# Optimization experiments

Hardware: AMD Instinct MI355X
Metric: run time of the kernel (lower is better)

Reference implementation:

```python
import jax, jax.numpy as jnp
import numpy as np

D_MODEL = 1024
D_STATE = 16
BATCH = 4
SEQLEN = 4096


def setup_inputs() -> dict:
    key = jax.random.key(0)
    kx, kA, kB, kC = jax.random.split(key, 4)
    x = jax.random.normal(kx, (BATCH, SEQLEN, D_MODEL), dtype=jnp.float32)
    # Params per init_weights(): A ~ N(-0.5, 0.1), B ~ N(0, 0.1), C ~ N(0, 0.1), D = 0
    A = -0.5 + 0.1 * jax.random.normal(kA, (1, D_STATE), dtype=jnp.float32)
    B_in = 0.1 * jax.random.normal(kB, (D_MODEL, D_STATE), dtype=jnp.float32)
    C = 0.1 * jax.random.normal(kC, (D_STATE, D_MODEL), dtype=jnp.float32)
    D = jnp.zeros((D_MODEL,), dtype=jnp.float32)
    return {"x": x, "A": A, "B_in": B_in, "C": C, "D": D}


def reference(x, A, B_in, C, D):
    # x: [B, N, E]; A: [1, S]; B_in: [E, S]; C: [S, E]; D: [E]
    A_neg = -jnp.exp(A)                              # [1, S]
    Bx = jnp.einsum('bne,es->bns', x, B_in)          # [B, N, S] = x @ B
    delta = jax.nn.softplus(Bx)                      # softplus(u @ B)
    decay = jnp.exp(delta * A_neg)                   # [B, N, S]

    def step(h, inp):
        d_t, bx_t = inp                              # each [B, S]
        h = h * d_t + bx_t
        return h, h

    h0 = jnp.zeros((x.shape[0], A.shape[1]), dtype=x.dtype)
    # scan over time: inputs [N, B, S]
    _, hs = jax.lax.scan(step, h0, (decay.transpose(1, 0, 2), Bx.transpose(1, 0, 2)))
    # readout: y_t = h_t @ C + x_t * D  (dropout p=0.0 -> identity)
    y = jnp.einsum('nbs,se->bne', hs, C) + x * D
    return y
```

## Files before the change

kernel.cpp:

```cpp
#include <hip/hip_runtime.h>

#define NSEQ 4096
#define EDIM 1024

#define OFF_BXT  0u
#define OFF_DECT 262144u
#define OFF_HT   524288u

__device__ __forceinline__ void fma4(float4& a, float xv, const float4& b) {
    a.x = fmaf(xv, b.x, a.x);
    a.y = fmaf(xv, b.y, a.y);
    a.z = fmaf(xv, b.z, a.z);
    a.w = fmaf(xv, b.w, a.w);
}

__global__ __launch_bounds__(512) void k1_bx(const float* __restrict__ x,
                                             const float* __restrict__ A,
                                             const float* __restrict__ Bin,
                                             float* __restrict__ ws) {
    __shared__ float smem[8704];

    const int tid  = threadIdx.x;
    const int lane = tid & 63;
    const int wu   = __builtin_amdgcn_readfirstlane(tid) >> 6;
    const int r0   = blockIdx.x * 64;
    const int b    = r0 >> 12;
    const int n0   = r0 & 4095;

    const float4* xf4 = (const float4*)x;
    const float4* Bf4 = (const float4*)Bin;

    float acc[16];
#pragma unroll
    for (int s = 0; s < 16; s++) acc[s] = 0.f;

    float4 pf[4];
#pragma unroll
    for (int k = 0; k < 4; k++) {
        int i = tid + 512 * k, row = i >> 5, c4 = i & 31;
        pf[k] = xf4[(size_t)(r0 + row) * 256 + c4];
    }

    for (int c = 0; c < 8; ++c) {
        if (c) __syncthreads();
#pragma unroll
        for (int k = 0; k < 4; k++) {
            int i = tid + 512 * k, row = i >> 5, c4 = i & 31;
            float* p = &smem[row * 129 + c4 * 4];
            p[0] = pf[k].x; p[1] = pf[k].y; p[2] = pf[k].z; p[3] = pf[k].w;
        }
        if (c < 7) {
#pragma unroll
            for (int k = 0; k < 4; k++) {
                int i = tid + 512 * k, row = i >> 5, c4 = i & 31;
                pf[k] = xf4[(size_t)(r0 + row) * 256 + (c + 1) * 32 + c4];
            }
        }
        __syncthreads();

        const int eb = wu * 16;
#pragma unroll
        for (int j = 0; j < 16; ++j) {
            const int e = c * 128 + eb + j;
            const float4 b0 = Bf4[e * 4 + 0];
            const float4 b1 = Bf4[e * 4 + 1];
            const float4 b2 = Bf4[e * 4 + 2];
            const float4 b3 = Bf4[e * 4 + 3];
            const float xv = smem[lane * 129 + eb + j];
            acc[0]  = fmaf(xv, b0.x, acc[0]);  acc[1]  = fmaf(xv, b0.y, acc[1]);
            acc[2]  = fmaf(xv, b0.z, acc[2]);  acc[3]  = fmaf(xv, b0.w, acc[3]);
            acc[4]  = fmaf(xv, b1.x, acc[4]);  acc[5]  = fmaf(xv, b1.y, acc[5]);
            acc[6]  = fmaf(xv, b1.z, acc[6]);  acc[7]  = fmaf(xv, b1.w, acc[7]);
            acc[8]  = fmaf(xv, b2.x, acc[8]);  acc[9]  = fmaf(xv, b2.y, acc[9]);
            acc[10] = fmaf(xv, b2.z, acc[10]); acc[11] = fmaf(xv, b2.w, acc[11]);
            acc[12] = fmaf(xv, b3.x, acc[12]); acc[13] = fmaf(xv, b3.y, acc[13]);
            acc[14] = fmaf(xv, b3.z, acc[14]); acc[15] = fmaf(xv, b3.w, acc[15]);
        }
    }

    __syncthreads();
    {
        int base = (wu * 64 + lane) * 17;
#pragma unroll
        for (int s = 0; s < 16; s++) smem[base + s] = acc[s];
    }
    __syncthreads();

#pragma unroll
    for (int half = 0; half < 2; half++) {
        int o   = tid + half * 512;
        int s   = o >> 6;
        int row = o & 63;
        float v = 0.f;
#pragma unroll
        for (int w = 0; w < 8; w++) v += smem[(w * 64 + row) * 17 + s];
        float sp  = fmaxf(v, 0.f) + log1pf(expf(-fabsf(v)));
        float dec = expf(-expf(A[s]) * sp);
        size_t off = (size_t)(b * 16 + s) * NSEQ + n0 + row;
        ws[OFF_BXT + off]  = v;
        ws[OFF_DECT + off] = dec;
    }
}

__global__ __launch_bounds__(256) void k2_scan(float* __restrict__ ws) {
    __shared__ float sP[256], sH[256];
    const int tid   = threadIdx.x;
    const int chain = blockIdx.x;
    const size_t f4 = (size_t)chain * 1024 + tid * 4;

    const float4* Bx4 = (const float4*)(ws + OFF_BXT);
    const float4* De4 = (const float4*)(ws + OFF_DECT);
    float4 bx[4], de[4];
#pragma unroll
    for (int k = 0; k < 4; k++) { bx[k] = Bx4[f4 + k]; de[k] = De4[f4 + k]; }

    float P = 1.f, h = 0.f;
#pragma unroll
    for (int k = 0; k < 4; k++) {
        h = fmaf(h, de[k].x, bx[k].x); P *= de[k].x;
        h = fmaf(h, de[k].y, bx[k].y); P *= de[k].y;
        h = fmaf(h, de[k].z, bx[k].z); P *= de[k].z;
        h = fmaf(h, de[k].w, bx[k].w); P *= de[k].w;
    }

    sP[tid] = P; sH[tid] = h;
    __syncthreads();
    for (int off = 1; off < 256; off <<= 1) {
        float pp = 1.f, hp = 0.f;
        bool act = (tid >= off);
        if (act) { pp = sP[tid - off]; hp = sH[tid - off]; }
        float p = sP[tid], hh = sH[tid];
        __syncthreads();
        if (act) { sP[tid] = pp * p; sH[tid] = fmaf(hp, p, hh); }
        __syncthreads();
    }
    float hr = (tid > 0) ? sH[tid - 1] : 0.f;

    const int bb = chain >> 4, ss = chain & 15;
    float* ht = ws + OFF_HT + ((size_t)bb * NSEQ + tid * 16) * 16 + ss;
#pragma unroll
    for (int k = 0; k < 4; k++) {
        hr = fmaf(hr, de[k].x, bx[k].x); ht[(k * 4 + 0) * 16] = hr;
        hr = fmaf(hr, de[k].y, bx[k].y); ht[(k * 4 + 1) * 16] = hr;
        hr = fmaf(hr, de[k].z, bx[k].z); ht[(k * 4 + 2) * 16] = hr;
        hr = fmaf(hr, de[k].w, bx[k].w); ht[(k * 4 + 3) * 16] = hr;
    }
}

__global__ __launch_bounds__(256) void k3_out(const float* __restrict__ x,
                                              const float* __restrict__ C,
                                              const float* __restrict__ D,
                                              const float* __restrict__ ws,
                                              float* __restrict__ out) {
    const int tid = threadIdx.x;
    const int blk = blockIdx.x;
    const int tc  = blk & 255;
    const int b   = blk >> 8;
    const int t0  = tc * 16;

    const float4* C4 = (const float4*)C;
    float4 creg[16];
#pragma unroll
    for (int s = 0; s < 16; s++) creg[s] = C4[s * 256 + tid];
    float4 dreg = ((const float4*)D)[tid];

    const bool needX = __any((dreg.x != 0.f) | (dreg.y != 0.f) |
                             (dreg.z != 0.f) | (dreg.w != 0.f));

    const float* hb = ws + OFF_HT + ((size_t)b * NSEQ + t0) * 16;

    const float4* x4 = (const float4*)x;
    float4* o4 = (float4*)out;
    const size_t rowbase = ((size_t)b * NSEQ + t0) * 256;

    if (needX) {
#pragma unroll 4
        for (int tt = 0; tt < 16; tt++) {
            float4 xv = x4[rowbase + tt * 256 + tid];
            float4 y;
            y.x = xv.x * dreg.x; y.y = xv.y * dreg.y;
            y.z = xv.z * dreg.z; y.w = xv.w * dreg.w;
#pragma unroll
            for (int s = 0; s < 16; s++) fma4(y, hb[tt * 16 + s], creg[s]);
            o4[rowbase + tt * 256 + tid] = y;
        }
    } else {
#pragma unroll 4
        for (int tt = 0; tt < 16; tt++) {
            float4 y = make_float4(0.f, 0.f, 0.f, 0.f);
#pragma unroll
            for (int s = 0; s < 16; s++) fma4(y, hb[tt * 16 + s], creg[s]);
            o4[rowbase + tt * 256 + tid] = y;
        }
    }
}

extern "C" void kernel_launch(void* const* d_in, const int* in_sizes, int n_in,
                              void* d_out, int out_size, void* d_ws, size_t ws_size,
                              hipStream_t stream) {
    const float* x   = (const float*)d_in[0];
    const float* A   = (const float*)d_in[1];
    const float* Bin = (const float*)d_in[2];
    const float* C   = (const float*)d_in[3];
    const float* D   = (const float*)d_in[4];
    float* out = (float*)d_out;
    float* ws  = (float*)d_ws;

    hipLaunchKernelGGL(k1_bx,   dim3(256),  dim3(512), 0, stream, x, A, Bin, ws);
    hipLaunchKernelGGL(k2_scan, dim3(64),   dim3(256), 0, stream, ws);
    hipLaunchKernelGGL(k3_out,  dim3(1024), dim3(256), 0, stream, x, C, D, ws, out);
}
```

Before: 148.3 us.

## Split Bx GEMM over E halves, move softplus/decay into scan, shuffle-based scan

k1 now launches 512 blocks of 256 threads, each handling half of the E dimension for 64 rows. It uses double-buffered shared-memory staging with float4 stores and loads, and writes partial Bx sums to two workspace halves. k2 sums the halves, computes softplus and decay itself, and replaces the shared-memory Hillis-Steele scan with wave shuffles plus a small cross-wave combine, cutting the number of barriers. The aim is more parallelism in k1 and fewer barriers in k2, at the cost of an extra partial-sum write and read.

```diff
diff --git a/kernel.cpp b/kernel.cpp
--- a/kernel.cpp
+++ b/kernel.cpp
@@ -3,9 +3,8 @@
 #define NSEQ 4096
 #define EDIM 1024
 
-#define OFF_BXT  0u
-#define OFF_DECT 262144u
-#define OFF_HT   524288u
+#define OFF_PBX 0u
+#define OFF_HT  524288u
 
 __device__ __forceinline__ void fma4(float4& a, float xv, const float4& b) {
     a.x = fmaf(xv, b.x, a.x);
@@ -14,16 +13,16 @@
     a.w = fmaf(xv, b.w, a.w);
 }
 
-__global__ __launch_bounds__(512) void k1_bx(const float* __restrict__ x,
-                                             const float* __restrict__ A,
-                                             const float* __restrict__ Bin,
-                                             float* __restrict__ ws) {
-    __shared__ float smem[8704];
+__global__ __launch_bounds__(256, 2) void k1_bx(const float* __restrict__ x,
+                                                const float* __restrict__ Bin,
+                                                float* __restrict__ ws) {
+    __shared__ float smem[2 * 64 * 132];
 
     const int tid  = threadIdx.x;
     const int lane = tid & 63;
     const int wu   = __builtin_amdgcn_readfirstlane(tid) >> 6;
-    const int r0   = blockIdx.x * 64;
+    const int r0   = (blockIdx.x >> 1) * 64;
+    const int eh   = blockIdx.x & 1;
     const int b    = r0 >> 12;
     const int n0   = r0 & 4095;
 
@@ -34,116 +33,127 @@
 #pragma unroll
     for (int s = 0; s < 16; s++) acc[s] = 0.f;
 
-    float4 pf[4];
+    float4 pf[8];
+#pragma unroll
+    for (int k = 0; k < 8; k++) {
+        int i = tid + 256 * k, row = i >> 5, c4 = i & 31;
+        pf[k] = xf4[(size_t)(r0 + row) * 256 + eh * 128 + c4];
+    }
+
+    for (int c = 0; c < 4; ++c) {
+        float* stg = &smem[(c & 1) * 8448];
+#pragma unroll
+        for (int k = 0; k < 8; k++) {
+            int i = tid + 256 * k, row = i >> 5, c4 = i & 31;
+            *(float4*)&stg[row * 132 + c4 * 4] = pf[k];
+        }
+        if (c < 3) {
+#pragma unroll
+            for (int k = 0; k < 8; k++) {
+                int i = tid + 256 * k, row = i >> 5, c4 = i & 31;
+                pf[k] = xf4[(size_t)(r0 + row) * 256 + eh * 128 + (c + 1) * 32 + c4];
+            }
+        }
+        __syncthreads();
+
+#pragma unroll
+        for (int j4 = 0; j4 < 8; j4++) {
+            const float4 xq = *(const float4*)&stg[lane * 132 + wu * 32 + j4 * 4];
+#pragma unroll
+            for (int jj = 0; jj < 4; jj++) {
+                const int e = eh * 512 + c * 128 + wu * 32 + j4 * 4 + jj;
+                const float4 b0 = Bf4[e * 4 + 0];
+                const float4 b1 = Bf4[e * 4 + 1];
+                const float4 b2 = Bf4[e * 4 + 2];
+                const float4 b3 = Bf4[e * 4 + 3];
+                const float xv = (jj == 0) ? xq.x : (jj == 1) ? xq.y
+                                : (jj == 2) ? xq.z : xq.w;
+                acc[0]  = fmaf(xv, b0.x, acc[0]);  acc[1]  = fmaf(xv, b0.y, acc[1]);
+                acc[2]  = fmaf(xv, b0.z, acc[2]);  acc[3]  = fmaf(xv, b0.w, acc[3]);
+                acc[4]  = fmaf(xv, b1.x, acc[4]);  acc[5]  = fmaf(xv, b1.y, acc[5]);
+                acc[6]  = fmaf(xv, b1.z, acc[6]);  acc[7]  = fmaf(xv, b1.w, acc[7]);
+                acc[8]  = fmaf(xv, b2.x, acc[8]);  acc[9]  = fmaf(xv, b2.y, acc[9]);
+                acc[10] = fmaf(xv, b2.z, acc[10]); acc[11] = fmaf(xv, b2.w, acc[11]);
+                acc[12] = fmaf(xv, b3.x, acc[12]); acc[13] = fmaf(xv, b3.y, acc[13]);
+                acc[14] = fmaf(xv, b3.z, acc[14]); acc[15] = fmaf(xv, b3.w, acc[15]);
+            }
+        }
+        __syncthreads();
+    }
+
+    {
+        const int rb = (wu * 64 + lane) * 17;
+#pragma unroll
+        for (int s = 0; s < 16; s++) smem[rb + s] = acc[s];
+    }
+    __syncthreads();
+
+#pragma unroll
+    for (int q = 0; q < 4; q++) {
+        const int o   = tid + 256 * q;
+        const int s   = o >> 6;
+        const int row = o & 63;
+        const float v = smem[(0 * 64 + row) * 17 + s] + smem[(1 * 64 + row) * 17 + s] +
+                        smem[(2 * 64 + row) * 17 + s] + smem[(3 * 64 + row) * 17 + s];
+        ws[OFF_PBX + eh * 262144u + (size_t)(b * 16 + s) * NSEQ + n0 + row] = v;
+    }
+}
+
+__global__ __launch_bounds__(256) void k2_scan(const float* __restrict__ A,
+                                               float* __restrict__ ws) {
+    __shared__ float sP[4], sH[4];
+    const int tid   = threadIdx.x;
+    const int lane  = tid & 63;
+    const int w     = tid >> 6;
+    const int chain = blockIdx.x;
+    const int bb    = chain >> 4, ss = chain & 15;
+
+    const float4* P0 = (const float4*)(ws + OFF_PBX) + (size_t)chain * 1024;
+    const float4* P1 = (const float4*)(ws + OFF_PBX + 262144u) + (size_t)chain * 1024;
+
+    float bx[16], de[16];
+    const float Ae = expf(A[ss]);
 #pragma unroll
     for (int k = 0; k < 4; k++) {
-        int i = tid + 512 * k, row = i >> 5, c4 = i & 31;
-        pf[k] = xf4[(size_t)(r0 + row) * 256 + c4];
-    }
-
-    for (int c = 0; c < 8; ++c) {
-        if (c) __syncthreads();
-#pragma unroll
-        for (int k = 0; k < 4; k++) {
-            int i = tid + 512 * k, row = i >> 5, c4 = i & 31;
-            float* p = &smem[row * 129 + c4 * 4];
-            p[0] = pf[k].x; p[1] = pf[k].y; p[2] = pf[k].z; p[3] = pf[k].w;
-        }
-        if (c < 7) {
-#pragma unroll
-            for (int k = 0; k < 4; k++) {
-                int i = tid + 512 * k, row = i >> 5, c4 = i & 31;
-                pf[k] = xf4[(size_t)(r0 + row) * 256 + (c + 1) * 32 + c4];
-            }
-        }
-        __syncthreads();
-
-        const int eb = wu * 16;
-#pragma unroll
-        for (int j = 0; j < 16; ++j) {
-            const int e = c * 128 + eb + j;
-            const float4 b0 = Bf4[e * 4 + 0];
-            const float4 b1 = Bf4[e * 4 + 1];
-            const float4 b2 = Bf4[e * 4 + 2];
-            const float4 b3 = Bf4[e * 4 + 3];
-            const float xv = smem[lane * 129 + eb + j];
-            acc[0]  = fmaf(xv, b0.x, acc[0]);  acc[1]  = fmaf(xv, b0.y, acc[1]);
-            acc[2]  = fmaf(xv, b0.z, acc[2]);  acc[3]  = fmaf(xv, b0.w, acc[3]);
-            acc[4]  = fmaf(xv, b1.x, acc[4]);  acc[5]  = fmaf(xv, b1.y, acc[5]);
-            acc[6]  = fmaf(xv, b1.z, acc[6]);  acc[7]  = fmaf(xv, b1.w, acc[7]);
-            acc[8]  = fmaf(xv, b2.x, acc[8]);  acc[9]  = fmaf(xv, b2.y, acc[9]);
-            acc[10] = fmaf(xv, b2.z, acc[10]); acc[11] = fmaf(xv, b2.w, acc[11]);
-            acc[12] = fmaf(xv, b3.x, acc[12]); acc[13] = fmaf(xv, b3.y, acc[13]);
-            acc[14] = fmaf(xv, b3.z, acc[14]); acc[15] = fmaf(xv, b3.w, acc[15]);
-        }
-    }
-
+        float4 a0 = P0[tid * 4 + k], a1 = P1[tid * 4 + k];
+        float vv[4] = {a0.x + a1.x, a0.y + a1.y, a0.z + a1.z, a0.w + a1.w};
+#pragma unroll
+        for (int j = 0; j < 4; j++) {
+            float v  = vv[j];
+            float sp = fmaxf(v, 0.f) + log1pf(expf(-fabsf(v)));
+            bx[k * 4 + j] = v;
+            de[k * 4 + j] = expf(-Ae * sp);
+        }
+    }
+
+    float P = 1.f, h = 0.f;
+#pragma unroll
+    for (int k = 0; k < 16; k++) { h = fmaf(h, de[k], bx[k]); P *= de[k]; }
+
+    float Pi = P, hi = h;
+#pragma unroll
+    for (int off = 1; off < 64; off <<= 1) {
+        float Pp = __shfl_up(Pi, off, 64);
+        float hp = __shfl_up(hi, off, 64);
+        if (lane >= off) { hi = fmaf(hp, Pi, hi); Pi *= Pp; }
+    }
+
+    if (lane == 63) { sP[w] = Pi; sH[w] = hi; }
     __syncthreads();
-    {
-        int base = (wu * 64 + lane) * 17;
-#pragma unroll
-        for (int s = 0; s < 16; s++) smem[base + s] = acc[s];
-    }
-    __syncthreads();
-
-#pragma unroll
-    for (int half = 0; half < 2; half++) {
-        int o   = tid + half * 512;
-        int s   = o >> 6;
-        int row = o & 63;
-        float v = 0.f;
-#pragma unroll
-        for (int w = 0; w < 8; w++) v += smem[(w * 64 + row) * 17 + s];
-        float sp  = fmaxf(v, 0.f) + log1pf(expf(-fabsf(v)));
-        float dec = expf(-expf(A[s]) * sp);
-        size_t off = (size_t)(b * 16 + s) * NSEQ + n0 + row;
-        ws[OFF_BXT + off]  = v;
-        ws[OFF_DECT + off] = dec;
-    }
-}
-
-__global__ __launch_bounds__(256) void k2_scan(float* __restrict__ ws) {
-    __shared__ float sP[256], sH[256];
-    const int tid   = threadIdx.x;
-    const int chain = blockIdx.x;
-    const size_t f4 = (size_t)chain * 1024 + tid * 4;
-
-    const float4* Bx4 = (const float4*)(ws + OFF_BXT);
-    const float4* De4 = (const float4*)(ws + OFF_DECT);
-    float4 bx[4], de[4];
-#pragma unroll
-    for (int k = 0; k < 4; k++) { bx[k] = Bx4[f4 + k]; de[k] = De4[f4 + k]; }
-
-    float P = 1.f, h = 0.f;
-#pragma unroll
-    for (int k = 0; k < 4; k++) {
-        h = fmaf(h, de[k].x, bx[k].x); P *= de[k].x;
-        h = fmaf(h, de[k].y, bx[k].y); P *= de[k].y;
-        h = fmaf(h, de[k].z, bx[k].z); P *= de[k].z;
-        h = fmaf(h, de[k].w, bx[k].w); P *= de[k].w;
-    }
-
-    sP[tid] = P; sH[tid] = h;
-    __syncthreads();
-    for (int off = 1; off < 256; off <<= 1) {
-        float pp = 1.f, hp = 0.f;
-        bool act = (tid >= off);
-        if (act) { pp = sP[tid - off]; hp = sH[tid - off]; }
-        float p = sP[tid], hh = sH[tid];
-        __syncthreads();
-        if (act) { sP[tid] = pp * p; sH[tid] = fmaf(hp, p, hh); }
-        __syncthreads();
-    }
-    float hr = (tid > 0) ? sH[tid - 1] : 0.f;
-
-    const int bb = chain >> 4, ss = chain & 15;
-    float* ht = ws + OFF_HT + ((size_t)bb * NSEQ + tid * 16) * 16 + ss;
-#pragma unroll
-    for (int k = 0; k < 4; k++) {
-        hr = fmaf(hr, de[k].x, bx[k].x); ht[(k * 4 + 0) * 16] = hr;
-        hr = fmaf(hr, de[k].y, bx[k].y); ht[(k * 4 + 1) * 16] = hr;
-        hr = fmaf(hr, de[k].z, bx[k].z); ht[(k * 4 + 2) * 16] = hr;
-        hr = fmaf(hr, de[k].w, bx[k].w); ht[(k * 4 + 3) * 16] = hr;
+
+    float hw = 0.f;
+    for (int q = 0; q < w; q++) hw = fmaf(hw, sP[q], sH[q]);
+
+    float Pe = __shfl_up(Pi, 1, 64);
+    float he = __shfl_up(hi, 1, 64);
+    if (lane == 0) { Pe = 1.f; he = 0.f; }
+    float hr = fmaf(hw, Pe, he);
+
+    float* htp = ws + OFF_HT + ((size_t)bb * NSEQ + tid * 16) * 16 + ss;
+#pragma unroll
+    for (int k = 0; k < 16; k++) {
+        hr = fmaf(hr, de[k], bx[k]);
+        htp[k * 16] = hr;
     }
 }
 
@@ -206,7 +216,7 @@
     float* out = (float*)d_out;
     float* ws  = (float*)d_ws;
 
-    hipLaunchKernelGGL(k1_bx,   dim3(256),  dim3(512), 0, stream, x, A, Bin, ws);
-    hipLaunchKernelGGL(k2_scan, dim3(64),   dim3(256), 0, stream, ws);
+    hipLaunchKernelGGL(k1_bx,   dim3(512),  dim3(256), 0, stream, x, Bin, ws);
+    hipLaunchKernelGGL(k2_scan, dim3(64),   dim3(256), 0, stream, A, ws);
     hipLaunchKernelGGL(k3_out,  dim3(1024), dim3(256), 0, stream, x, C, D, ws, out);
 }
```

Result: slower. 162.0 us (+9.2%).
